# Optimization experiments

Measured on AMD Instinct MI355X. Metric: run time of the kernel, lower is better.

Reference implementation:

```python
import jax, jax.numpy as jnp
import numpy as np

CHANNELS = 256
CODEBOOK_SIZE = 8192
UPDATE_SPEED = 0.01
N_TOKENS = 32768


def setup_inputs() -> dict:
    key = jax.random.key(0)
    k1, k2 = jax.random.split(key)
    embeddings = jax.random.normal(k1, (N_TOKENS, CHANNELS), dtype=jnp.float32)
    code_usage = jnp.ones((CODEBOOK_SIZE,), dtype=jnp.float32)
    code_embedding_sum = jax.random.normal(k2, (CODEBOOK_SIZE, CHANNELS), dtype=jnp.float32)
    return {"embeddings": embeddings, "code_usage": code_usage,
            "code_embedding_sum": code_embedding_sum}


def reference(embeddings, code_usage, code_embedding_sum):
    # codebook from EMA statistics: [K, C]
    codebook = code_embedding_sum / jnp.clip(code_usage, 1e-5, None)[:, None]

    # encode: nearest code by Euclidean distance. argmin over codes is
    # invariant under sqrt, so use squared distances (avoids sqrt of [K, N]).
    cb_sq = jnp.sum(codebook * codebook, axis=-1)            # [K]
    x_sq = jnp.sum(embeddings * embeddings, axis=-1)         # [N]
    # d2[k, n] = ||cb_k - x_n||^2
    d2 = cb_sq[:, None] - 2.0 * jnp.einsum('kc,nc->kn', codebook, embeddings) + x_sq[None, :]
    codes = jnp.argmin(d2, axis=0).astype(jnp.int32)         # [N]

    # decode: gather codebook rows
    quantized = jnp.take(codebook, codes, axis=0)            # [N, C]

    # straight-through estimator
    embeddings_q = embeddings + jax.lax.stop_gradient(quantized - embeddings)

    # commitment loss: mse(stop_grad(embeddings_q), embeddings)
    diff = jax.lax.stop_gradient(embeddings_q) - embeddings
    commitment_loss = jnp.mean(diff * diff)

    # EMA updates (training mode, under no_grad in the original)
    n = embeddings.shape[0]
    counts = jax.ops.segment_sum(jnp.ones((n,), dtype=code_usage.dtype),
                                 codes, num_segments=CODEBOOK_SIZE)
    emb_sum = jax.ops.segment_sum(embeddings, codes, num_segments=CODEBOOK_SIZE)
    s = jnp.float32(UPDATE_SPEED)
    new_code_usage = jax.lax.stop_gradient(code_usage * (1.0 - s) + counts * s)
    new_code_embedding_sum = jax.lax.stop_gradient(
        code_embedding_sum * (1.0 - s) + emb_sum * s)

    return codes, embeddings_q, commitment_loss, new_code_usage, new_code_embedding_sum
```

## Files before the change

### kernel.cpp

```cpp
#include <hip/hip_runtime.h>

#define CH 256
#define KC 8192
#define KCP 8448
#define NT 32768

#define TM 128
#define TN 128
#define BK 32
#define YS 3
#define JQ (KCP / YS)
#define NSTG ((JQ / TN) * (CH / BK))

typedef _Float16 half4_t __attribute__((ext_vector_type(4)));
typedef _Float16 half8_t __attribute__((ext_vector_type(8)));
typedef float floatx4 __attribute__((ext_vector_type(4)));

typedef __attribute__((address_space(1))) const unsigned int guint_t;
typedef __attribute__((address_space(3))) unsigned int luint_t;

__device__ __forceinline__ int swz(int row, int chunk) {
    return row * BK + ((chunk ^ ((row >> 1) & 3)) << 3);
}

__global__ void k_prep(const float* __restrict__ usage,
                       const float* __restrict__ ces,
                       const float* __restrict__ emb,
                       _Float16* __restrict__ cbh,
                       _Float16* __restrict__ cbl,
                       float* __restrict__ cbsq,
                       _Float16* __restrict__ eh,
                       _Float16* __restrict__ el,
                       int* __restrict__ hist,
                       unsigned long long* __restrict__ packed) {
    int b = blockIdx.x, t = threadIdx.x;
    if (b < KCP) {
        if (b < KC) {
            float uc = fmaxf(usage[b], 1e-5f);
            float v  = ces[b * CH + t];
            float cb = v / uc;
            _Float16 h = (_Float16)cb;
            cbh[b * CH + t] = h;
            cbl[b * CH + t] = (_Float16)(cb - (float)h);

            float p = cb * cb;
            #pragma unroll
            for (int off = 32; off; off >>= 1) p += __shfl_down(p, off);
            __shared__ float ps[4];
            int lane = t & 63, w = t >> 6;
            if (lane == 0) ps[w] = p;
            __syncthreads();
            if (t == 0) cbsq[b] = ps[0] + ps[1] + ps[2] + ps[3];
            if (t == 1) hist[b] = 0;
            int gid = b * CH + t;
            if (gid < NT) packed[gid] = 0xFFFFFFFFFFFFFFFFull;
        } else {
            cbh[b * CH + t] = (_Float16)0.0f;
            cbl[b * CH + t] = (_Float16)0.0f;
            if (t == 0) cbsq[b] = 3.0e38f;
        }
    } else {
        int i = (b - KCP) * 256 + t;
        float4 v = ((const float4*)emb)[i];
        float va[4] = {v.x, v.y, v.z, v.w};
        half4_t h, l;
        #pragma unroll
        for (int q = 0; q < 4; ++q) {
            _Float16 hh = (_Float16)va[q];
            h[q] = hh;
            l[q] = (_Float16)(va[q] - (float)hh);
        }
        ((half4_t*)eh)[i] = h;
        ((half4_t*)el)[i] = l;
    }
}

__launch_bounds__(256, 3)
__global__ void k_argmin(const _Float16* __restrict__ eh,
                         const _Float16* __restrict__ el,
                         const _Float16* __restrict__ cbh,
                         const _Float16* __restrict__ cbl,
                         const float* __restrict__ cbsq,
                         unsigned long long* __restrict__ packed) {
    __shared__ __align__(16) _Float16 sm[4][TM * BK];
    __shared__ float cand_v[2][TM];
    __shared__ int   cand_i[2][TM];

    const int t    = threadIdx.x;
    const int lane = t & 63;
    const int wave = t >> 6;
    const int wx   = wave & 1;
    const int wy   = wave >> 1;
    const int lr   = lane & 15;
    const int koq  = lane >> 4;

    const int n0 = blockIdx.x * TM;
    const int jq = blockIdx.y * JQ;

    const _Float16* dsrc = (wave == 0) ? eh : (wave == 1) ? el
                         : (wave == 2) ? cbh : cbl;
    const int qsw   = (lane & 3) ^ ((lane >> 3) & 3);
    const int lrow  = lane >> 2;

    float minv[16];
    int   mini[16];
    #pragma unroll
    for (int e = 0; e < 16; ++e) { minv[e] = 3.402823466e38f; mini[e] = 0; }

    floatx4 acc[4][4];
    #pragma unroll
    for (int mf = 0; mf < 4; ++mf)
        #pragma unroll
        for (int nf = 0; nf < 4; ++nf)
            acc[mf][nf] = (floatx4){0.f, 0.f, 0.f, 0.f};

    #pragma unroll 1
    for (int s = 0; s < NSTG; ++s) {
        const int c0 = (s & 7) * BK;
        const int jb = jq + (s >> 3) * TN;
        const int rb = (wave < 2) ? n0 : jb;

        {
            const _Float16* gbase = dsrc + (size_t)(rb + lrow) * CH + c0 + qsw * 8;
            #pragma unroll
            for (int i = 0; i < 8; ++i) {
                const _Float16* g = gbase + (size_t)(i * 16) * CH;
                __builtin_amdgcn_global_load_lds(
                    (guint_t*)g, (luint_t*)&sm[wave][i * 512], 16, 0, 0);
            }
        }
        __syncthreads();

        half8_t fah[4], fal[4];
        #pragma unroll
        for (int mf = 0; mf < 4; ++mf) {
            int off = swz(wy * 64 + mf * 16 + lr, koq);
            fah[mf] = *(const half8_t*)&sm[0][off];
            fal[mf] = *(const half8_t*)&sm[1][off];
        }
        #pragma unroll
        for (int nf = 0; nf < 4; ++nf) {
            int offb = swz(wx * 64 + nf * 16 + lr, koq);
            half8_t fbh = *(const half8_t*)&sm[2][offb];
            half8_t fbl = *(const half8_t*)&sm[3][offb];
            #pragma unroll
            for (int mf = 0; mf < 4; ++mf) {
                acc[mf][nf] = __builtin_amdgcn_mfma_f32_16x16x32_f16(
                    fah[mf], fbh, acc[mf][nf], 0, 0, 0);
                acc[mf][nf] = __builtin_amdgcn_mfma_f32_16x16x32_f16(
                    fah[mf], fbl, acc[mf][nf], 0, 0, 0);
                acc[mf][nf] = __builtin_amdgcn_mfma_f32_16x16x32_f16(
                    fal[mf], fbh, acc[mf][nf], 0, 0, 0);
            }
        }

        if ((s & 7) == 7) {
            int jbase = jq + (s >> 3) * TN;
            #pragma unroll
            for (int nf = 0; nf < 4; ++nf) {
                int j = jbase + wx * 64 + nf * 16 + lr;
                float sq = cbsq[j];
                #pragma unroll
                for (int mf = 0; mf < 4; ++mf) {
                    floatx4 a = acc[mf][nf];
                    #pragma unroll
                    for (int r = 0; r < 4; ++r) {
                        float sc = sq - 2.0f * a[r];
                        int e = mf * 4 + r;
                        if (sc < minv[e]) { minv[e] = sc; mini[e] = j; }
                    }
                    acc[mf][nf] = (floatx4){0.f, 0.f, 0.f, 0.f};
                }
            }
        }
        __syncthreads();
    }

    #pragma unroll
    for (int e = 0; e < 16; ++e) {
        float v = minv[e];
        int   x = mini[e];
        #pragma unroll
        for (int m = 1; m <= 8; m <<= 1) {
            float ov = __shfl_xor(v, m, 64);
            int   ox = __shfl_xor(x, m, 64);
            if (ov < v || (ov == v && ox < x)) { v = ov; x = ox; }
        }
        if (lr == 0) {
            int row = wy * 64 + (e >> 2) * 16 + (lane >> 4) * 4 + (e & 3);
            cand_v[wx][row] = v;
            cand_i[wx][row] = x;
        }
    }
    __syncthreads();

    if (t < TM) {
        float v0 = cand_v[0][t]; int i0 = cand_i[0][t];
        float v1 = cand_v[1][t]; int i1 = cand_i[1][t];
        if (v1 < v0 || (v1 == v0 && i1 < i0)) { v0 = v1; i0 = i1; }
        unsigned sb = __float_as_uint(v0);
        sb = (sb & 0x80000000u) ? ~sb : (sb | 0x80000000u);
        unsigned long long key = ((unsigned long long)sb << 32) | (unsigned)i0;
        atomicMin(&packed[n0 + t], key);
    }
}

__global__ void k_gather(const float* __restrict__ emb,
                         const float* __restrict__ ces,
                         const float* __restrict__ usage,
                         const unsigned long long* __restrict__ packed,
                         float* __restrict__ out_eq,
                         float* __restrict__ codes_f,
                         int* __restrict__ hist,
                         float* __restrict__ partials) {
    int t = threadIdx.x;
    int wave = t >> 6, lane = t & 63;
    int n = blockIdx.x * 4 + wave;
    int k = (int)(packed[n] & 0xFFFFFFFFull);
    float uc = fmaxf(usage[k], 1e-5f);
    int c = lane * 4;

    float4 e = *(const float4*)&emb[(size_t)n * CH + c];
    float4 v = *(const float4*)&ces[(size_t)k * CH + c];
    float ea[4] = {e.x, e.y, e.z, e.w};
    float va[4] = {v.x, v.y, v.z, v.w};
    float eqa[4];
    float p = 0.0f;
    #pragma unroll
    for (int q = 0; q < 4; ++q) {
        float cb = va[q] / uc;
        float eq = ea[q] + (cb - ea[q]);
        eqa[q] = eq;
        float d = eq - ea[q];
        p += d * d;
    }
    *(float4*)&out_eq[(size_t)n * CH + c] =
        (float4){eqa[0], eqa[1], eqa[2], eqa[3]};

    #pragma unroll
    for (int off = 32; off; off >>= 1) p += __shfl_down(p, off);
    __shared__ float ps[4];
    if (lane == 0) {
        ps[wave] = p;
        codes_f[n] = (float)k;
        atomicAdd(&hist[k], 1);
    }
    __syncthreads();
    if (t == 0) partials[blockIdx.x] = ps[0] + ps[1] + ps[2] + ps[3];
}

__global__ void k_scan(const int* __restrict__ hist,
                       int* __restrict__ offs,
                       int* __restrict__ cursor) {
    __shared__ int bs[256];
    int t = threadIdx.x;
    int base = t * 32;
    int loc[32];
    int s = 0;
    #pragma unroll
    for (int i = 0; i < 32; ++i) { loc[i] = s; s += hist[base + i]; }
    int mysum = s;
    bs[t] = s;
    __syncthreads();
    for (int off = 1; off < 256; off <<= 1) {
        int v = (t >= off) ? bs[t - off] : 0;
        __syncthreads();
        bs[t] += v;
        __syncthreads();
    }
    int excl = bs[t] - mysum;
    #pragma unroll
    for (int i = 0; i < 32; ++i) {
        int o = excl + loc[i];
        offs[base + i]   = o;
        cursor[base + i] = o;
    }
}

__global__ void k_scatter(const unsigned long long* __restrict__ packed,
                          int* __restrict__ cursor,
                          int* __restrict__ bucket) {
    int n = blockIdx.x * 256 + threadIdx.x;
    int k = (int)(packed[n] & 0xFFFFFFFFull);
    int pos = atomicAdd(&cursor[k], 1);
    bucket[pos] = n;
}

__global__ void k_ema(const float* __restrict__ emb,
                      const float* __restrict__ ces,
                      const float* __restrict__ usage,
                      const int* __restrict__ hist,
                      const int* __restrict__ offs,
                      const int* __restrict__ bucket,
                      float* __restrict__ out_ces,
                      float* __restrict__ out_usage) {
    const float s = 0.01f;
    const float oms = 1.0f - s;
    int k = blockIdx.x, t = threadIdx.x;
    int start = offs[k], cnt = hist[k];
    float sum = 0.0f;
    #pragma unroll 2
    for (int i = 0; i < cnt; ++i) {
        int n = bucket[start + i];
        sum += emb[(size_t)n * CH + t];
    }
    out_ces[(size_t)k * CH + t] = oms * ces[(size_t)k * CH + t] + s * sum;
    if (t == 0) out_usage[k] = oms * usage[k] + s * (float)cnt;
}

__global__ void k_final(const float* __restrict__ partials,
                        float* __restrict__ out_loss) {
    int t = threadIdx.x;
    float p = 0.0f;
    for (int i = t; i < NT / 4; i += 256) p += partials[i];
    #pragma unroll
    for (int off = 32; off; off >>= 1) p += __shfl_down(p, off);
    __shared__ float ps[4];
    if ((t & 63) == 0) ps[t >> 6] = p;
    __syncthreads();
    if (t == 0)
        out_loss[0] = (ps[0] + ps[1] + ps[2] + ps[3]) * (1.0f / 8388608.0f);
}

extern "C" void kernel_launch(void* const* d_in, const int* in_sizes, int n_in,
                              void* d_out, int out_size, void* d_ws, size_t ws_size,
                              hipStream_t stream) {
    const float* emb   = (const float*)d_in[0];
    const float* usage = (const float*)d_in[1];
    const float* ces   = (const float*)d_in[2];

    float* out      = (float*)d_out;
    float* o_codes  = out;
    float* o_eq     = out + NT;
    float* o_loss   = o_eq + (size_t)NT * CH;
    float* o_usage  = o_loss + 1;
    float* o_ces    = o_usage + KC;

    unsigned long long* packed = (unsigned long long*)d_ws;
    float* cbsq     = (float*)(packed + NT);
    float* partials = cbsq + KCP;
    int* hist   = (int*)(partials + NT / 4);
    int* offs   = hist + KC;
    int* cursor = offs + KC;
    int* bucket = cursor + KC;
    _Float16* eh  = (_Float16*)(bucket + NT);
    _Float16* el  = eh + (size_t)NT * CH;
    _Float16* cbh = el + (size_t)NT * CH;
    _Float16* cbl = cbh + (size_t)KCP * CH;

    k_prep<<<KCP + NT * CH / 1024, 256, 0, stream>>>(
        usage, ces, emb, cbh, cbl, cbsq, eh, el, hist, packed);
    dim3 agrid(NT / TM, YS);
    k_argmin<<<agrid, 256, 0, stream>>>(eh, el, cbh, cbl, cbsq, packed);
    k_gather<<<NT / 4, 256, 0, stream>>>(emb, ces, usage, packed, o_eq,
                                         o_codes, hist, partials);
    k_scan<<<1, 256, 0, stream>>>(hist, offs, cursor);
    k_scatter<<<NT / 256, 256, 0, stream>>>(packed, cursor, bucket);
    k_ema<<<KC, 256, 0, stream>>>(emb, ces, usage, hist, offs, bucket,
                                  o_ces, o_usage);
    k_final<<<1, 256, 0, stream>>>(partials, o_loss);
}
```

Measured before the change: 625.7 us.

## Double-buffer LDS tiles in argmin GEMM to overlap global loads with MFMA

```diff
diff --git a/kernel.cpp b/kernel.cpp
--- a/kernel.cpp
+++ b/kernel.cpp
@@ -75,14 +75,14 @@
     }
 }
 
-__launch_bounds__(256, 3)
+__launch_bounds__(256, 2)
 __global__ void k_argmin(const _Float16* __restrict__ eh,
                          const _Float16* __restrict__ el,
                          const _Float16* __restrict__ cbh,
                          const _Float16* __restrict__ cbl,
                          const float* __restrict__ cbsq,
                          unsigned long long* __restrict__ packed) {
-    __shared__ __align__(16) _Float16 sm[4][TM * BK];
+    __shared__ __align__(16) _Float16 sm[2][4][TM * BK];
     __shared__ float cand_v[2][TM];
     __shared__ int   cand_i[2][TM];
 
@@ -114,35 +114,47 @@
         for (int nf = 0; nf < 4; ++nf)
             acc[mf][nf] = (floatx4){0.f, 0.f, 0.f, 0.f};
 
+    auto dma = [&](int buf, int sg) {
+        const int c0 = (sg & 7) * BK;
+        const int jb = jq + (sg >> 3) * TN;
+        const int rb = (wave < 2) ? n0 : jb;
+        const _Float16* gbase = dsrc + (size_t)(rb + lrow) * CH + c0 + qsw * 8;
+        #pragma unroll
+        for (int i = 0; i < 8; ++i) {
+            const _Float16* g = gbase + (size_t)(i * 16) * CH;
+            __builtin_amdgcn_global_load_lds(
+                (guint_t*)g, (luint_t*)&sm[buf][wave][i * 512], 16, 0, 0);
+        }
+    };
+
+    dma(0, 0);
+
     #pragma unroll 1
     for (int s = 0; s < NSTG; ++s) {
-        const int c0 = (s & 7) * BK;
-        const int jb = jq + (s >> 3) * TN;
-        const int rb = (wave < 2) ? n0 : jb;
-
-        {
-            const _Float16* gbase = dsrc + (size_t)(rb + lrow) * CH + c0 + qsw * 8;
-            #pragma unroll
-            for (int i = 0; i < 8; ++i) {
-                const _Float16* g = gbase + (size_t)(i * 16) * CH;
-                __builtin_amdgcn_global_load_lds(
-                    (guint_t*)g, (luint_t*)&sm[wave][i * 512], 16, 0, 0);
-            }
-        }
-        __syncthreads();
+        const int cur = s & 1;
+
+        if (s + 1 < NSTG) {
+            dma(cur ^ 1, s + 1);
+            asm volatile("s_waitcnt vmcnt(8)" ::: "memory");
+        } else {
+            asm volatile("s_waitcnt vmcnt(0)" ::: "memory");
+        }
+        __builtin_amdgcn_s_barrier();
+        __builtin_amdgcn_sched_barrier(0);
 
         half8_t fah[4], fal[4];
         #pragma unroll
         for (int mf = 0; mf < 4; ++mf) {
             int off = swz(wy * 64 + mf * 16 + lr, koq);
-            fah[mf] = *(const half8_t*)&sm[0][off];
-            fal[mf] = *(const half8_t*)&sm[1][off];
-        }
+            fah[mf] = *(const half8_t*)&sm[cur][0][off];
+            fal[mf] = *(const half8_t*)&sm[cur][1][off];
+        }
+        __builtin_amdgcn_s_setprio(1);
         #pragma unroll
         for (int nf = 0; nf < 4; ++nf) {
             int offb = swz(wx * 64 + nf * 16 + lr, koq);
-            half8_t fbh = *(const half8_t*)&sm[2][offb];
-            half8_t fbl = *(const half8_t*)&sm[3][offb];
+            half8_t fbh = *(const half8_t*)&sm[cur][2][offb];
+            half8_t fbl = *(const half8_t*)&sm[cur][3][offb];
             #pragma unroll
             for (int mf = 0; mf < 4; ++mf) {
                 acc[mf][nf] = __builtin_amdgcn_mfma_f32_16x16x32_f16(
@@ -153,6 +165,7 @@
                     fal[mf], fbh, acc[mf][nf], 0, 0, 0);
             }
         }
+        __builtin_amdgcn_s_setprio(0);
 
         if ((s & 7) == 7) {
             int jbase = jq + (s >> 3) * TN;
@@ -173,7 +186,10 @@
                 }
             }
         }
-        __syncthreads();
+
+        asm volatile("s_waitcnt lgkmcnt(0)" ::: "memory");
+        __builtin_amdgcn_sched_barrier(0);
+        __builtin_amdgcn_s_barrier();
     }
 
     #pragma unroll
```

New measurement: 706.9 us. +13.0%, slower.

## Restructure argmin GEMM: register-resident tokens, double-buffered codebook LDS, 32x32 MFMA

Applied to the files above, without the earlier changes.

```diff
diff --git a/kernel.cpp b/kernel.cpp
--- a/kernel.cpp
+++ b/kernel.cpp
@@ -2,26 +2,18 @@
 
 #define CH 256
 #define KC 8192
-#define KCP 8448
 #define NT 32768
 
-#define TM 128
-#define TN 128
-#define BK 32
-#define YS 3
-#define JQ (KCP / YS)
-#define NSTG ((JQ / TN) * (CH / BK))
+#define TPW 32
+#define JT  64
+#define JTS 64
 
 typedef _Float16 half4_t __attribute__((ext_vector_type(4)));
 typedef _Float16 half8_t __attribute__((ext_vector_type(8)));
-typedef float floatx4 __attribute__((ext_vector_type(4)));
+typedef float floatx16 __attribute__((ext_vector_type(16)));
 
 typedef __attribute__((address_space(1))) const unsigned int guint_t;
 typedef __attribute__((address_space(3))) unsigned int luint_t;
-
-__device__ __forceinline__ int swz(int row, int chunk) {
-    return row * BK + ((chunk ^ ((row >> 1) & 3)) << 3);
-}
 
 __global__ void k_prep(const float* __restrict__ usage,
                        const float* __restrict__ ces,
@@ -34,33 +26,27 @@
                        int* __restrict__ hist,
                        unsigned long long* __restrict__ packed) {
     int b = blockIdx.x, t = threadIdx.x;
-    if (b < KCP) {
-        if (b < KC) {
-            float uc = fmaxf(usage[b], 1e-5f);
-            float v  = ces[b * CH + t];
-            float cb = v / uc;
-            _Float16 h = (_Float16)cb;
-            cbh[b * CH + t] = h;
-            cbl[b * CH + t] = (_Float16)(cb - (float)h);
-
-            float p = cb * cb;
-            #pragma unroll
-            for (int off = 32; off; off >>= 1) p += __shfl_down(p, off);
-            __shared__ float ps[4];
-            int lane = t & 63, w = t >> 6;
-            if (lane == 0) ps[w] = p;
-            __syncthreads();
-            if (t == 0) cbsq[b] = ps[0] + ps[1] + ps[2] + ps[3];
-            if (t == 1) hist[b] = 0;
-            int gid = b * CH + t;
-            if (gid < NT) packed[gid] = 0xFFFFFFFFFFFFFFFFull;
-        } else {
-            cbh[b * CH + t] = (_Float16)0.0f;
-            cbl[b * CH + t] = (_Float16)0.0f;
-            if (t == 0) cbsq[b] = 3.0e38f;
-        }
+    if (b < KC) {
+        float uc = fmaxf(usage[b], 1e-5f);
+        float v  = ces[b * CH + t];
+        float cb = v / uc;
+        _Float16 h = (_Float16)cb;
+        cbh[b * CH + t] = h;
+        cbl[b * CH + t] = (_Float16)(cb - (float)h);
+
+        float p = cb * cb;
+        #pragma unroll
+        for (int off = 32; off; off >>= 1) p += __shfl_down(p, off);
+        __shared__ float ps[4];
+        int lane = t & 63, w = t >> 6;
+        if (lane == 0) ps[w] = p;
+        __syncthreads();
+        if (t == 0) cbsq[b] = ps[0] + ps[1] + ps[2] + ps[3];
+        if (t == 1) hist[b] = 0;
+        int gid = b * CH + t;
+        if (gid < NT) packed[gid] = 0xFFFFFFFFFFFFFFFFull;
     } else {
-        int i = (b - KCP) * 256 + t;
+        int i = (b - KC) * 256 + t;
         float4 v = ((const float4*)emb)[i];
         float va[4] = {v.x, v.y, v.z, v.w};
         half4_t h, l;
@@ -75,133 +61,125 @@
     }
 }
 
-__launch_bounds__(256, 3)
+__launch_bounds__(512, 2)
 __global__ void k_argmin(const _Float16* __restrict__ eh,
                          const _Float16* __restrict__ el,
                          const _Float16* __restrict__ cbh,
                          const _Float16* __restrict__ cbl,
                          const float* __restrict__ cbsq,
                          unsigned long long* __restrict__ packed) {
-    __shared__ __align__(16) _Float16 sm[4][TM * BK];
-    __shared__ float cand_v[2][TM];
-    __shared__ int   cand_i[2][TM];
+    __shared__ __align__(16) char smB[131072];
 
     const int t    = threadIdx.x;
     const int lane = t & 63;
     const int wave = t >> 6;
-    const int wx   = wave & 1;
-    const int wy   = wave >> 1;
-    const int lr   = lane & 15;
-    const int koq  = lane >> 4;
-
-    const int n0 = blockIdx.x * TM;
-    const int jq = blockIdx.y * JQ;
-
-    const _Float16* dsrc = (wave == 0) ? eh : (wave == 1) ? el
-                         : (wave == 2) ? cbh : cbl;
-    const int qsw   = (lane & 3) ^ ((lane >> 3) & 3);
-    const int lrow  = lane >> 2;
+    const int lr32 = lane & 31;
+    const int kh   = lane >> 5;
+
+    const int n0w = blockIdx.x * 256 + wave * TPW;
+    const int jq  = blockIdx.y * (JTS * JT);
+
+    half8_t aregh[16], aregl[16];
+    {
+        const size_t rowoff = (size_t)(n0w + lr32) * CH + kh * 8;
+        #pragma unroll
+        for (int ks = 0; ks < 16; ++ks) {
+            aregh[ks] = *(const half8_t*)(eh + rowoff + ks * 16);
+            aregl[ks] = *(const half8_t*)(el + rowoff + ks * 16);
+        }
+    }
+
+    auto dmaB = [&](int buf, int jt) {
+        const int jb = jq + jt * JT;
+        #pragma unroll
+        for (int d = 0; d < 8; ++d) {
+            const int p   = wave * 4 + (d >> 1);
+            const int ks  = p >> 1;
+            const int h   = p & 1;
+            const int sub = d & 1;
+            const _Float16* src = h ? cbl : cbh;
+            const _Float16* g = src + (size_t)(jb + lane) * CH
+                              + ks * 16 + sub * 8;
+            __builtin_amdgcn_global_load_lds(
+                (guint_t*)g,
+                (luint_t*)(smB + buf * 65536 + ks * 4096 + h * 2048
+                           + sub * 1024),
+                16, 0, 0);
+        }
+    };
 
     float minv[16];
     int   mini[16];
     #pragma unroll
     for (int e = 0; e < 16; ++e) { minv[e] = 3.402823466e38f; mini[e] = 0; }
 
-    floatx4 acc[4][4];
-    #pragma unroll
-    for (int mf = 0; mf < 4; ++mf)
-        #pragma unroll
-        for (int nf = 0; nf < 4; ++nf)
-            acc[mf][nf] = (floatx4){0.f, 0.f, 0.f, 0.f};
+    floatx16 acc0, acc1;
+    #pragma unroll
+    for (int r = 0; r < 16; ++r) { acc0[r] = 0.f; acc1[r] = 0.f; }
+
+    dmaB(0, 0);
+    __syncthreads();
+
+    const int lslot = (kh * 64 + lr32) * 16;
 
     #pragma unroll 1
-    for (int s = 0; s < NSTG; ++s) {
-        const int c0 = (s & 7) * BK;
-        const int jb = jq + (s >> 3) * TN;
-        const int rb = (wave < 2) ? n0 : jb;
-
-        {
-            const _Float16* gbase = dsrc + (size_t)(rb + lrow) * CH + c0 + qsw * 8;
-            #pragma unroll
-            for (int i = 0; i < 8; ++i) {
-                const _Float16* g = gbase + (size_t)(i * 16) * CH;
-                __builtin_amdgcn_global_load_lds(
-                    (guint_t*)g, (luint_t*)&sm[wave][i * 512], 16, 0, 0);
-            }
-        }
+    for (int jt = 0; jt < JTS; ++jt) {
+        const int buf = jt & 1;
+        const int jb  = jq + jt * JT;
+
+        if (jt + 1 < JTS) dmaB(buf ^ 1, jt + 1);
+
+        const float csq0 = cbsq[jb + lr32];
+        const float csq1 = cbsq[jb + 32 + lr32];
+
+        const char* bbase = smB + buf * 65536 + lslot;
+        #pragma unroll
+        for (int ks = 0; ks < 16; ++ks) {
+            const char* bp = bbase + ks * 4096;
+            half8_t fbh0 = *(const half8_t*)(bp);
+            half8_t fbh1 = *(const half8_t*)(bp + 512);
+            half8_t fbl0 = *(const half8_t*)(bp + 2048);
+            half8_t fbl1 = *(const half8_t*)(bp + 2560);
+            acc0 = __builtin_amdgcn_mfma_f32_32x32x16_f16(aregh[ks], fbh0, acc0, 0, 0, 0);
+            acc1 = __builtin_amdgcn_mfma_f32_32x32x16_f16(aregh[ks], fbh1, acc1, 0, 0, 0);
+            acc0 = __builtin_amdgcn_mfma_f32_32x32x16_f16(aregh[ks], fbl0, acc0, 0, 0, 0);
+            acc1 = __builtin_amdgcn_mfma_f32_32x32x16_f16(aregh[ks], fbl1, acc1, 0, 0, 0);
+            acc0 = __builtin_amdgcn_mfma_f32_32x32x16_f16(aregl[ks], fbh0, acc0, 0, 0, 0);
+            acc1 = __builtin_amdgcn_mfma_f32_32x32x16_f16(aregl[ks], fbh1, acc1, 0, 0, 0);
+        }
+
+        #pragma unroll
+        for (int r = 0; r < 16; ++r) {
+            float s0 = csq0 - 2.0f * acc0[r];
+            float s1 = csq1 - 2.0f * acc1[r];
+            float sv = s0; int si = jb + lr32;
+            if (s1 < sv) { sv = s1; si = jb + 32 + lr32; }
+            if (sv < minv[r]) { minv[r] = sv; mini[r] = si; }
+            acc0[r] = 0.f;
+            acc1[r] = 0.f;
+        }
+
         __syncthreads();
-
-        half8_t fah[4], fal[4];
-        #pragma unroll
-        for (int mf = 0; mf < 4; ++mf) {
-            int off = swz(wy * 64 + mf * 16 + lr, koq);
-            fah[mf] = *(const half8_t*)&sm[0][off];
-            fal[mf] = *(const half8_t*)&sm[1][off];
-        }
-        #pragma unroll
-        for (int nf = 0; nf < 4; ++nf) {
-            int offb = swz(wx * 64 + nf * 16 + lr, koq);
-            half8_t fbh = *(const half8_t*)&sm[2][offb];
-            half8_t fbl = *(const half8_t*)&sm[3][offb];
-            #pragma unroll
-            for (int mf = 0; mf < 4; ++mf) {
-                acc[mf][nf] = __builtin_amdgcn_mfma_f32_16x16x32_f16(
-                    fah[mf], fbh, acc[mf][nf], 0, 0, 0);
-                acc[mf][nf] = __builtin_amdgcn_mfma_f32_16x16x32_f16(
-                    fah[mf], fbl, acc[mf][nf], 0, 0, 0);
-                acc[mf][nf] = __builtin_amdgcn_mfma_f32_16x16x32_f16(
-                    fal[mf], fbh, acc[mf][nf], 0, 0, 0);
-            }
-        }
-
-        if ((s & 7) == 7) {
-            int jbase = jq + (s >> 3) * TN;
-            #pragma unroll
-            for (int nf = 0; nf < 4; ++nf) {
-                int j = jbase + wx * 64 + nf * 16 + lr;
-                float sq = cbsq[j];
-                #pragma unroll
-                for (int mf = 0; mf < 4; ++mf) {
-                    floatx4 a = acc[mf][nf];
-                    #pragma unroll
-                    for (int r = 0; r < 4; ++r) {
-                        float sc = sq - 2.0f * a[r];
-                        int e = mf * 4 + r;
-                        if (sc < minv[e]) { minv[e] = sc; mini[e] = j; }
-                    }
-                    acc[mf][nf] = (floatx4){0.f, 0.f, 0.f, 0.f};
-                }
-            }
-        }
-        __syncthreads();
-    }
-
-    #pragma unroll
-    for (int e = 0; e < 16; ++e) {
-        float v = minv[e];
-        int   x = mini[e];
-        #pragma unroll
-        for (int m = 1; m <= 8; m <<= 1) {
+    }
+
+    #pragma unroll
+    for (int r = 0; r < 16; ++r) {
+        float v = minv[r];
+        int   x = mini[r];
+        #pragma unroll
+        for (int m = 1; m <= 16; m <<= 1) {
             float ov = __shfl_xor(v, m, 64);
             int   ox = __shfl_xor(x, m, 64);
             if (ov < v || (ov == v && ox < x)) { v = ov; x = ox; }
         }
-        if (lr == 0) {
-            int row = wy * 64 + (e >> 2) * 16 + (lane >> 4) * 4 + (e & 3);
-            cand_v[wx][row] = v;
-            cand_i[wx][row] = x;
-        }
-    }
-    __syncthreads();
-
-    if (t < TM) {
-        float v0 = cand_v[0][t]; int i0 = cand_i[0][t];
-        float v1 = cand_v[1][t]; int i1 = cand_i[1][t];
-        if (v1 < v0 || (v1 == v0 && i1 < i0)) { v0 = v1; i0 = i1; }
-        unsigned sb = __float_as_uint(v0);
-        sb = (sb & 0x80000000u) ? ~sb : (sb | 0x80000000u);
-        unsigned long long key = ((unsigned long long)sb << 32) | (unsigned)i0;
-        atomicMin(&packed[n0 + t], key);
+        if (lr32 == 0) {
+            int tok = n0w + (r & 3) + 8 * (r >> 2) + 4 * kh;
+            unsigned sb = __float_as_uint(v);
+            sb = (sb & 0x80000000u) ? ~sb : (sb | 0x80000000u);
+            unsigned long long key =
+                ((unsigned long long)sb << 32) | (unsigned)x;
+            atomicMin(&packed[tok], key);
+        }
     }
 }
 
@@ -338,7 +316,7 @@
 
     unsigned long long* packed = (unsigned long long*)d_ws;
     float* cbsq     = (float*)(packed + NT);
-    float* partials = cbsq + KCP;
+    float* partials = cbsq + KC;
     int* hist   = (int*)(partials + NT / 4);
     int* offs   = hist + KC;
     int* cursor = offs + KC;
@@ -346,12 +324,12 @@
     _Float16* eh  = (_Float16*)(bucket + NT);
     _Float16* el  = eh + (size_t)NT * CH;
     _Float16* cbh = el + (size_t)NT * CH;
-    _Float16* cbl = cbh + (size_t)KCP * CH;
-
-    k_prep<<<KCP + NT * CH / 1024, 256, 0, stream>>>(
+    _Float16* cbl = cbh + (size_t)KC * CH;
+
+    k_prep<<<KC + NT * CH / 1024, 256, 0, stream>>>(
         usage, ces, emb, cbh, cbl, cbsq, eh, el, hist, packed);
-    dim3 agrid(NT / TM, YS);
-    k_argmin<<<agrid, 256, 0, stream>>>(eh, el, cbh, cbl, cbsq, packed);
+    dim3 agrid(NT / 256, 2);
+    k_argmin<<<agrid, 512, 0, stream>>>(eh, el, cbh, cbl, cbsq, packed);
     k_gather<<<NT / 4, 256, 0, stream>>>(emb, ces, usage, packed, o_eq,
                                          o_codes, hist, partials);
     k_scan<<<1, 256, 0, stream>>>(hist, offs, cursor);
```

Measured after the change: 578.8 us. 7.5% less time.
